# Kernel tuning notes

Measured on AMD Instinct MI355X. Metric: run time of the kernel, lower is better.

## Reference

```python
import jax, jax.numpy as jnp
import numpy as np

TEMPERATURE = 0.5


def _cos_sim_flat(a, b):
    # row-normalize then full similarity matrix, flattened (matches torch.mm(a_n, b_n.T).flatten())
    a_n = a / jnp.linalg.norm(a, axis=1, keepdims=True)
    b_n = b / jnp.linalg.norm(b, axis=1, keepdims=True)
    return (a_n @ b_n.T).reshape(-1)


def setup_inputs() -> dict:
    key = jax.random.key(0)
    k1, k2, k3 = jax.random.split(key, 3)
    N, D = 4096, 2048
    return {
        "x_source": jax.random.normal(k1, (N, D), dtype=jnp.float32),
        "x_bc_target": jax.random.normal(k2, (N, D), dtype=jnp.float32),
        "x_raw_target": jax.random.normal(k3, (N, D), dtype=jnp.float32),
    }


def reference(x_source, x_bc_target, x_raw_target):
    sim_pos = _cos_sim_flat(x_source, x_bc_target)  # [N*N]
    sim_neg = _cos_sim_flat(x_source, x_raw_target)  # [N*N]
    # denom = sum_j exp(sim_neg_j / T); loss_i = -log(exp(sim_pos_i/T)/denom)
    # = -sim_pos_i/T + logsumexp(sim_neg/T); mean over i. Same math as the
    # original scalar loops, computed as one fused reduction.
    log_denom = jax.nn.logsumexp(sim_neg / TEMPERATURE)
    cl_loss = jnp.mean(log_denom - sim_pos / TEMPERATURE)
    return cl_loss
```

## Files before the change

### kernel.cpp

```cpp
#include <hip/hip_runtime.h>
#include <hip/hip_bf16.h>

#define NR 4096
#define DD 2048
#define INV_T 2.0f
#define QSCALE 32.0f
#define ACC_TO_LOGIT (INV_T / (QSCALE * QSCALE))
#define QS4 64.0f
#define ACC4_TO_LOGIT (INV_T / (QS4 * QS4))

typedef __attribute__((ext_vector_type(2))) float floatx2;
typedef __attribute__((ext_vector_type(4))) float floatx4;
typedef __attribute__((ext_vector_type(4))) int int4v;
typedef __attribute__((ext_vector_type(8))) int int8v;

static __device__ __forceinline__ void async_copy16(const void* g, void* lds) {
  __builtin_amdgcn_global_load_lds((const __attribute__((address_space(1))) void*)g,
                                   (__attribute__((address_space(3))) void*)lds,
                                   16, 0, 0);
}

static __device__ __forceinline__ unsigned int enc4(float x) {
  float u = fminf(fabsf(x), 6.0f);
  int c = (u >= 0.25f) + (u >= 0.75f) + (u >= 1.25f) + (u >= 1.75f) +
          (u >= 2.5f) + (u >= 3.5f) + (u >= 5.0f);
  return (unsigned)(c | (x < 0.f ? 8 : 0));
}

static __device__ __forceinline__ unsigned int pack8_fp4(
    const float4& v0, const float4& v1, float s) {
  return enc4(v0.x * s)        | (enc4(v0.y * s) << 4)  |
         (enc4(v0.z * s) << 8) | (enc4(v0.w * s) << 12) |
         (enc4(v1.x * s) << 16)| (enc4(v1.y * s) << 20) |
         (enc4(v1.z * s) << 24)| (enc4(v1.w * s) << 28);
}

__global__ __launch_bounds__(256) void normalize_kernel(
    const float* __restrict__ src, const float* __restrict__ bc,
    const float* __restrict__ raw,
    unsigned char* __restrict__ a8row, unsigned int* __restrict__ a4,
    unsigned char* __restrict__ b8, unsigned int* __restrict__ c4,
    float* __restrict__ zbuf) {
  const int row = blockIdx.x;
  const int mat = blockIdx.y;
  const int tid = threadIdx.x;
  const float* base = (mat == 0) ? src : ((mat == 1) ? bc : raw);
  const float4* b4 = (const float4*)(base + (size_t)row * DD);

  if (mat == 1 && row < 17) {
    const int idx = row * 256 + tid;
    if (idx < 2 * DD + 1) zbuf[idx] = 0.f;
  }

  float4 v0 = b4[tid * 2];
  float4 v1 = b4[tid * 2 + 1];
  float ss = v0.x * v0.x + v0.y * v0.y + v0.z * v0.z + v0.w * v0.w +
             v1.x * v1.x + v1.y * v1.y + v1.z * v1.z + v1.w * v1.w;
  #pragma unroll
  for (int off = 32; off > 0; off >>= 1) ss += __shfl_down(ss, off, 64);

  __shared__ float sred[4];
  __shared__ float sinv;
  if ((tid & 63) == 0) sred[tid >> 6] = ss;
  __syncthreads();
  if (tid == 0) sinv = rsqrtf(sred[0] + sred[1] + sred[2] + sred[3]);
  __syncthreads();

  if (mat == 2) {
    c4[row * (DD / 8) + tid] = pack8_fp4(v0, v1, sinv * QS4);
    return;
  }

  const float s = sinv * QSCALE;
  int d0 = __builtin_amdgcn_cvt_pk_fp8_f32(v0.x * s, v0.y * s, 0, false);
  d0 = __builtin_amdgcn_cvt_pk_fp8_f32(v0.z * s, v0.w * s, d0, true);
  int d1 = __builtin_amdgcn_cvt_pk_fp8_f32(v1.x * s, v1.y * s, 0, false);
  d1 = __builtin_amdgcn_cvt_pk_fp8_f32(v1.z * s, v1.w * s, d1, true);
  int2 o; o.x = d0; o.y = d1;
  if (mat == 0) {
    *(int2*)(a8row + (size_t)row * DD + tid * 8) = o;
    a4[row * (DD / 8) + tid] = pack8_fp4(v0, v1, sinv * QS4);
  } else {
    *(int2*)(b8 + (size_t)row * DD + tid * 8) = o;
  }
}

__global__ __launch_bounds__(256, 2) void gemm_expsum_kernel(
    const unsigned char* __restrict__ a4, const unsigned char* __restrict__ c4,
    float* __restrict__ S_part) {
  __shared__ unsigned char As[2][128 * 128];
  __shared__ unsigned char Cs[2][128 * 128];
  const int tid = threadIdx.x;
  const int lane = tid & 63;
  const int wave = tid >> 6;
  const int wr = wave >> 1;
  const int wc = wave & 1;
  const int quad = lane >> 4;
  const int l16 = lane & 15;
  const int bc = blockIdx.x, br = blockIdx.y;

  floatx4 acc[4][4] = {};

  const int wrow = lane >> 3;
  const int csrc = (lane & 7) ^ (wrow & 7);
  const unsigned char* gA[4];
  const unsigned char* gC[4];
  int ldsOff[4];
  #pragma unroll
  for (int q = 0; q < 4; q++) {
    const int m = wave * 4 + q;
    const int row = m * 8 + wrow;
    gA[q] = a4 + (size_t)(br * 128 + row) * 1024 + csrc * 16;
    gC[q] = c4 + (size_t)(bc * 128 + row) * 1024 + csrc * 16;
    ldsOff[q] = m * 1024;
  }

  #pragma unroll
  for (int q = 0; q < 4; q++) {
    async_copy16(gA[q], &As[0][ldsOff[q]]);
    async_copy16(gC[q], &Cs[0][ldsOff[q]]);
    gA[q] += 128; gC[q] += 128;
  }

  const int NKT = DD / 256;
  #pragma unroll 2
  for (int kt = 0; kt < NKT; kt++) {
    const int cur = kt & 1;
    __syncthreads();

    if (kt < NKT - 1) {
      #pragma unroll
      for (int q = 0; q < 4; q++) {
        async_copy16(gA[q], &As[cur ^ 1][ldsOff[q]]);
        async_copy16(gC[q], &Cs[cur ^ 1][ldsOff[q]]);
        gA[q] += 128; gC[q] += 128;
      }
    }

    int4v af[2][4], bf[2][4];
    #pragma unroll
    for (int s = 0; s < 2; s++) {
      #pragma unroll
      for (int i = 0; i < 4; i++) {
        const int r = wr * 64 + i * 16 + l16;
        const int pc = (s * 4 + quad) ^ (r & 7);
        af[s][i] = *(const int4v*)&As[cur][r * 128 + pc * 16];
      }
      #pragma unroll
      for (int j = 0; j < 4; j++) {
        const int r = wc * 64 + j * 16 + l16;
        const int pc = (s * 4 + quad) ^ (r & 7);
        bf[s][j] = *(const int4v*)&Cs[cur][r * 128 + pc * 16];
      }
    }
    #pragma unroll
    for (int s = 0; s < 2; s++)
      #pragma unroll
      for (int i = 0; i < 4; i++) {
        const int8v a8v = int8v{af[s][i][0], af[s][i][1], af[s][i][2],
                                af[s][i][3], 0, 0, 0, 0};
        #pragma unroll
        for (int j = 0; j < 4; j++) {
          const int8v b8v = int8v{bf[s][j][0], bf[s][j][1], bf[s][j][2],
                                  bf[s][j][3], 0, 0, 0, 0};
          acc[i][j] = __builtin_amdgcn_mfma_scale_f32_16x16x128_f8f6f4(
              a8v, b8v, acc[i][j], 4 , 4 ,
              0, 0x7F7F7F7F, 0, 0x7F7F7F7F );
        }
      }
  }

  float local = 0.f;
  #pragma unroll
  for (int i = 0; i < 4; i++)
    #pragma unroll
    for (int j = 0; j < 4; j++)
      #pragma unroll
      for (int r = 0; r < 4; r++)
        local += __expf(acc[i][j][r] * ACC4_TO_LOGIT);
  #pragma unroll
  for (int off = 32; off > 0; off >>= 1) local += __shfl_down(local, off, 64);
  __shared__ float red[4];
  if (lane == 0) red[wave] = local;
  __syncthreads();
  if (tid == 0) S_part[br * 32 + bc] = red[0] + red[1] + red[2] + red[3];
}

__global__ __launch_bounds__(256) void colsum_finalize_kernel(
    const unsigned char* __restrict__ a8, const unsigned char* __restrict__ b8,
    float* __restrict__ s_a, float* __restrict__ s_b,
    float* __restrict__ counter, const float* __restrict__ S_part,
    float* __restrict__ out) {
  __shared__ float lds[32 * 264];
  const int tid = threadIdx.x;
  const int rt = tid >> 3;
  const int ct = tid & 7;
  const int cg = blockIdx.x & 7;
  const int rg = blockIdx.x >> 3;
  const int cbase = cg * 256 + ct * 32;
  const int rbase = rg * 256 + rt;

  float accA[32], accB[32];
  #pragma unroll
  for (int i = 0; i < 32; i++) { accA[i] = 0.f; accB[i] = 0.f; }

  #pragma unroll
  for (int k = 0; k < 8; k++) {
    const size_t off = (size_t)(rbase + k * 32) * DD + cbase;
    const int8v ra = *(const int8v*)(a8 + off);
    const int8v rb = *(const int8v*)(b8 + off);
    #pragma unroll
    for (int u = 0; u < 8; u++) {
      floatx2 lo = __builtin_amdgcn_cvt_pk_f32_fp8(ra[u], false);
      floatx2 hi = __builtin_amdgcn_cvt_pk_f32_fp8(ra[u], true);
      accA[u * 4 + 0] += lo[0]; accA[u * 4 + 1] += lo[1];
      accA[u * 4 + 2] += hi[0]; accA[u * 4 + 3] += hi[1];
      lo = __builtin_amdgcn_cvt_pk_f32_fp8(rb[u], false);
      hi = __builtin_amdgcn_cvt_pk_f32_fp8(rb[u], true);
      accB[u * 4 + 0] += lo[0]; accB[u * 4 + 1] += lo[1];
      accB[u * 4 + 2] += hi[0]; accB[u * 4 + 3] += hi[1];
    }
  }

  #pragma unroll
  for (int i = 0; i < 32; i += 4)
    *(floatx4*)&lds[rt * 264 + ct * 32 + i] =
        floatx4{accA[i], accA[i + 1], accA[i + 2], accA[i + 3]};
  __syncthreads();
  float sA = 0.f;
  #pragma unroll 8
  for (int r = 0; r < 32; r++) sA += lds[r * 264 + tid];
  atomicAdd(&s_a[cg * 256 + tid], sA);
  __syncthreads();

  #pragma unroll
  for (int i = 0; i < 32; i += 4)
    *(floatx4*)&lds[rt * 264 + ct * 32 + i] =
        floatx4{accB[i], accB[i + 1], accB[i + 2], accB[i + 3]};
  __syncthreads();
  float sB = 0.f;
  #pragma unroll 8
  for (int r = 0; r < 32; r++) sB += lds[r * 264 + tid];
  atomicAdd(&s_b[cg * 256 + tid], sB);

  __threadfence();
  __syncthreads();
  __shared__ bool amLast;
  if (tid == 0) amLast = (atomicAdd(counter, 1.0f) == 127.0f);
  __syncthreads();
  if (!amLast) return;
  __threadfence();

  float dot = 0.f;
  for (int d = tid; d < DD; d += 256)
    dot += atomicAdd(&s_a[d], 0.f) * atomicAdd(&s_b[d], 0.f);
  float se = 0.f;
  for (int i = tid; i < 1024; i += 256) se += S_part[i];

  #pragma unroll
  for (int off = 32; off > 0; off >>= 1) {
    dot += __shfl_down(dot, off, 64);
    se += __shfl_down(se, off, 64);
  }
  __shared__ float redd[4], reds[4];
  if ((tid & 63) == 0) { redd[tid >> 6] = dot; reds[tid >> 6] = se; }
  __syncthreads();
  if (tid == 0) {
    const float dt = redd[0] + redd[1] + redd[2] + redd[3];
    const float st = reds[0] + reds[1] + reds[2] + reds[3];
    out[0] = logf(st) - dt * (ACC_TO_LOGIT / ((float)NR * (float)NR));
  }
}

extern "C" void kernel_launch(void* const* d_in, const int* in_sizes, int n_in,
                              void* d_out, int out_size, void* d_ws, size_t ws_size,
                              hipStream_t stream) {
  const float* src = (const float*)d_in[0];
  const float* bc  = (const float*)d_in[1];
  const float* raw = (const float*)d_in[2];

  char* ws = (char*)d_ws;
  unsigned char* a8row = (unsigned char*)ws;
  unsigned char* b8 = (unsigned char*)(ws + (size_t)8 * 1024 * 1024);
  unsigned int* a4  = (unsigned int*)(ws + (size_t)16 * 1024 * 1024);
  unsigned int* c4  = (unsigned int*)(ws + (size_t)20 * 1024 * 1024);
  float* zbuf  = (float*)(ws + (size_t)24 * 1024 * 1024);
  float* s_a   = zbuf;
  float* s_b   = zbuf + DD;
  float* counter = zbuf + 2 * DD;
  float* S_part = (float*)(ws + (size_t)24 * 1024 * 1024 + 20480);

  normalize_kernel<<<dim3(NR, 3), 256, 0, stream>>>(src, bc, raw, a8row, a4,
                                                    b8, c4, zbuf);
  gemm_expsum_kernel<<<dim3(32, 32), 256, 0, stream>>>(
      (const unsigned char*)a4, (const unsigned char*)c4, S_part);
  colsum_finalize_kernel<<<128, 256, 0, stream>>>(a8row, b8, s_a, s_b, counter,
                                                  S_part, (float*)d_out);
}
```

Before: 166.1 us.

## Single-buffer GEMM LDS for higher occupancy, XCD-aware block swizzle, wider colsum grid

The FP4 GEMM drops double-buffered LDS for a single buffer with load-sync-compute-sync, halving LDS per block so three blocks can share a CU, and raises the launch-bounds occupancy hint to match. Block indices are remapped so that blocks on the same XCD cover a compact tile region for better L2 reuse. The column-sum kernel runs twice as many blocks, each covering half as many rows, with the last-block counter threshold updated. The cost is that global-to-LDS loads are no longer overlapped with MFMA work inside a block, so the scheme relies on other resident blocks to hide that latency.

```diff
diff --git a/kernel.cpp b/kernel.cpp
--- a/kernel.cpp
+++ b/kernel.cpp
@@ -85,11 +85,11 @@
   }
 }
 
-__global__ __launch_bounds__(256, 2) void gemm_expsum_kernel(
+__global__ __launch_bounds__(256, 3) void gemm_expsum_kernel(
     const unsigned char* __restrict__ a4, const unsigned char* __restrict__ c4,
     float* __restrict__ S_part) {
-  __shared__ unsigned char As[2][128 * 128];
-  __shared__ unsigned char Cs[2][128 * 128];
+  __shared__ unsigned char As[128 * 128];
+  __shared__ unsigned char Cs[128 * 128];
   const int tid = threadIdx.x;
   const int lane = tid & 63;
   const int wave = tid >> 6;
@@ -97,7 +97,11 @@
   const int wc = wave & 1;
   const int quad = lane >> 4;
   const int l16 = lane & 15;
-  const int bc = blockIdx.x, br = blockIdx.y;
+
+  const int flat = blockIdx.y * 32 + blockIdx.x;
+  const int xcd = flat & 7, slot = flat >> 3;
+  const int br = (xcd >> 1) * 8 + ((slot >> 3) & 7);
+  const int bc = (xcd & 1) * 16 + (slot >> 6) * 8 + (slot & 7);
 
   floatx4 acc[4][4] = {};
 
@@ -115,59 +119,46 @@
     ldsOff[q] = m * 1024;
   }
 
-  #pragma unroll
-  for (int q = 0; q < 4; q++) {
-    async_copy16(gA[q], &As[0][ldsOff[q]]);
-    async_copy16(gC[q], &Cs[0][ldsOff[q]]);
-    gA[q] += 128; gC[q] += 128;
-  }
-
   const int NKT = DD / 256;
-  #pragma unroll 2
   for (int kt = 0; kt < NKT; kt++) {
-    const int cur = kt & 1;
+    #pragma unroll
+    for (int q = 0; q < 4; q++) {
+      async_copy16(gA[q], &As[ldsOff[q]]);
+      async_copy16(gC[q], &Cs[ldsOff[q]]);
+      gA[q] += 128; gC[q] += 128;
+    }
     __syncthreads();
 
-    if (kt < NKT - 1) {
-      #pragma unroll
-      for (int q = 0; q < 4; q++) {
-        async_copy16(gA[q], &As[cur ^ 1][ldsOff[q]]);
-        async_copy16(gC[q], &Cs[cur ^ 1][ldsOff[q]]);
-        gA[q] += 128; gC[q] += 128;
-      }
-    }
-
-    int4v af[2][4], bf[2][4];
     #pragma unroll
     for (int s = 0; s < 2; s++) {
+      int4v af[4], bf[4];
       #pragma unroll
       for (int i = 0; i < 4; i++) {
         const int r = wr * 64 + i * 16 + l16;
         const int pc = (s * 4 + quad) ^ (r & 7);
-        af[s][i] = *(const int4v*)&As[cur][r * 128 + pc * 16];
+        af[i] = *(const int4v*)&As[r * 128 + pc * 16];
       }
       #pragma unroll
       for (int j = 0; j < 4; j++) {
         const int r = wc * 64 + j * 16 + l16;
         const int pc = (s * 4 + quad) ^ (r & 7);
-        bf[s][j] = *(const int4v*)&Cs[cur][r * 128 + pc * 16];
+        bf[j] = *(const int4v*)&Cs[r * 128 + pc * 16];
       }
-    }
-    #pragma unroll
-    for (int s = 0; s < 2; s++)
       #pragma unroll
       for (int i = 0; i < 4; i++) {
-        const int8v a8v = int8v{af[s][i][0], af[s][i][1], af[s][i][2],
-                                af[s][i][3], 0, 0, 0, 0};
+        const int8v a8v = int8v{af[i][0], af[i][1], af[i][2], af[i][3],
+                                0, 0, 0, 0};
         #pragma unroll
         for (int j = 0; j < 4; j++) {
-          const int8v b8v = int8v{bf[s][j][0], bf[s][j][1], bf[s][j][2],
-                                  bf[s][j][3], 0, 0, 0, 0};
+          const int8v b8v = int8v{bf[j][0], bf[j][1], bf[j][2], bf[j][3],
+                                  0, 0, 0, 0};
           acc[i][j] = __builtin_amdgcn_mfma_scale_f32_16x16x128_f8f6f4(
               a8v, b8v, acc[i][j], 4 , 4 ,
               0, 0x7F7F7F7F, 0, 0x7F7F7F7F );
         }
       }
+    }
+    __syncthreads();
   }
 
   float local = 0.f;
@@ -198,14 +189,14 @@
   const int cg = blockIdx.x & 7;
   const int rg = blockIdx.x >> 3;
   const int cbase = cg * 256 + ct * 32;
-  const int rbase = rg * 256 + rt;
+  const int rbase = rg * 128 + rt;
 
   float accA[32], accB[32];
   #pragma unroll
   for (int i = 0; i < 32; i++) { accA[i] = 0.f; accB[i] = 0.f; }
 
   #pragma unroll
-  for (int k = 0; k < 8; k++) {
+  for (int k = 0; k < 4; k++) {
     const size_t off = (size_t)(rbase + k * 32) * DD + cbase;
     const int8v ra = *(const int8v*)(a8 + off);
     const int8v rb = *(const int8v*)(b8 + off);
@@ -246,7 +237,7 @@
   __threadfence();
   __syncthreads();
   __shared__ bool amLast;
-  if (tid == 0) amLast = (atomicAdd(counter, 1.0f) == 127.0f);
+  if (tid == 0) amLast = (atomicAdd(counter, 1.0f) == 255.0f);
   __syncthreads();
   if (!amLast) return;
   __threadfence();
@@ -294,6 +285,6 @@
                                                     b8, c4, zbuf);
   gemm_expsum_kernel<<<dim3(32, 32), 256, 0, stream>>>(
       (const unsigned char*)a4, (const unsigned char*)c4, S_part);
-  colsum_finalize_kernel<<<128, 256, 0, stream>>>(a8row, b8, s_a, s_b, counter,
+  colsum_finalize_kernel<<<256, 256, 0, stream>>>(a8row, b8, s_a, s_b, counter,
                                                   S_part, (float*)d_out);
 }
```

Measured after the change: 170.7 us. +2.8%, slower.
